# Kernel tuning notes

Hardware: AMD Instinct MI355X
Metric: run time of the kernel (lower is better)

## Reference

```python
import jax, jax.numpy as jnp
import numpy as np

N_GRAPHS = 512
NODES_PER_G = 200
EDGES_PER_G = 6400
N = N_GRAPHS * NODES_PER_G        # 102400 nodes
E = N_GRAPHS * EDGES_PER_G        # 3276800 edges
HID = 128
NCLS = 10


def _linear_params(key, fan_in, fan_out):
    # torch nn.Linear default init: U(-1/sqrt(fan_in), 1/sqrt(fan_in))
    s = 1.0 / np.sqrt(fan_in)
    kw, kb = jax.random.split(key)
    W = jax.random.uniform(kw, (fan_in, fan_out), minval=-s, maxval=s, dtype=jnp.float32)
    b = jax.random.uniform(kb, (fan_out,), minval=-s, maxval=s, dtype=jnp.float32)
    return W, b


def setup_inputs() -> dict:
    key = jax.random.key(0)
    ks = jax.random.split(key, 10)
    # edges are confined within each graph (DGL batched graph structure)
    g_off = (jnp.arange(E, dtype=jnp.int32) // EDGES_PER_G) * NODES_PER_G
    src = (g_off + jax.random.randint(ks[0], (E,), 0, NODES_PER_G)).astype(jnp.int32)
    dst = (g_off + jax.random.randint(ks[1], (E,), 0, NODES_PER_G)).astype(jnp.int32)
    W1, b1 = _linear_params(ks[2], 1, HID)
    W2, b2 = _linear_params(ks[3], HID, HID)
    Wa, ba = _linear_params(ks[4], HID, 512)
    Wb, bb = _linear_params(ks[5], 512, 1024)
    Wc, bc = _linear_params(ks[6], 1024, 1024)
    Wd, bd = _linear_params(ks[7], 1024, 512)
    We, be = _linear_params(ks[8], 512, NCLS)
    return dict(src=src, dst=dst, W1=W1, b1=b1, W2=W2, b2=b2,
                Wa=Wa, ba=ba, Wb=Wb, bb=bb, Wc=Wc, bc=bc,
                Wd=Wd, bd=bd, We=We, be=be)


def reference(src, dst, W1, b1, W2, b2, Wa, ba, Wb, bb, Wc, bc, Wd, bd, We, be):
    seg = jax.ops.segment_sum
    ones = jnp.ones((E,), jnp.float32)
    in_deg = seg(ones, dst, num_segments=N)    # [N]
    out_deg = seg(ones, src, num_segments=N)   # [N]
    # DGL GraphConv norm='both': degrees clamped to min 1
    inv_out = (1.0 / jnp.sqrt(jnp.maximum(out_deg, 1.0)))[:, None]
    inv_in = (1.0 / jnp.sqrt(jnp.maximum(in_deg, 1.0)))[:, None]

    def gconv(h, W, b):
        h = (h @ W) * inv_out                    # src-side normalize (weight applied first; same math)
        h = seg(h[src], dst, num_segments=N)     # gather + scatter-add aggregation
        return h * inv_in + b                    # dst-side normalize + bias

    h = in_deg[:, None]                          # input node features = in-degrees, [N,1]
    h = jax.nn.relu(gconv(h, W1, b1))
    h = jax.nn.relu(gconv(h, W2, b2))

    gid = jnp.arange(N, dtype=jnp.int32) // NODES_PER_G
    hg = seg(h, gid, num_segments=N_GRAPHS) / float(NODES_PER_G)  # mean readout, [G,HID]

    x = jax.nn.relu(hg @ Wa + ba)
    x = jax.nn.relu(x @ Wb + bb)
    x = jax.nn.relu(x @ Wc + bc)
    x = jax.nn.relu(x @ Wd + bd)
    return jax.nn.softmax(x @ We + be, axis=-1)  # nn.Softmax over class dim
```

## Files before the change

### kernel.cpp

```cpp
#include <hip/hip_runtime.h>
#include <stdint.h>

typedef unsigned short u16;
typedef unsigned int   u32;

#define NG   512
#define NPG  200
#define EPG  6400
#define NN   (NG*NPG)
#define NE_  (NG*EPG)
#define HID  128
#define KP   224
#define AP   232
#define ZP   136
#define RQ   64
#define QCAP 2048

__device__ __forceinline__ float bf2f(u16 b){ u32 u = ((u32)b) << 16; return __builtin_bit_cast(float, u); }
__device__ __forceinline__ u16 f2bf(float f){
    u32 u = __builtin_bit_cast(u32, f);
    u = (u + 0x7FFFu + ((u >> 16) & 1u)) >> 16;
    return (u16)u;
}

typedef __attribute__((ext_vector_type(8))) short bf16x8;
typedef __attribute__((ext_vector_type(4))) float f32x4;

enum : int {
  O_W1 = 0,        O_b1 = 128,      O_W2 = 256,      O_b2 = 16640,
  O_Wa = 16768,    O_ba = 82304,    O_Wb = 82816,    O_bb = 607104,
  O_Wc = 608128,   O_bc = 1656704,  O_Wd = 1657728,  O_bd = 2182016,
  O_We = 2182528,  O_be = 2187648,  O_END = 2187658
};

__global__ __launch_bounds__(128) void k_detect(const u16* __restrict__ w1bits,
                                                int* __restrict__ flag)
{
    __shared__ int cnt;
    const int tid = threadIdx.x;
    if (tid == 0) cnt = 0;
    __syncthreads();
    u16 u = w1bits[tid];
    int e = (u >> 7) & 0xFF;
    if (e >= 0x7F) atomicAdd(&cnt, 1);
    __syncthreads();
    if (tid == 0) *flag = (cnt > 4) ? 1 : 0;
}

struct Cvt { const void* src[14]; int off[15]; };

__global__ __launch_bounds__(256) void k_convert(Cvt c, float* __restrict__ dst,
                                                 const int* __restrict__ flag, int total)
{
    const int f = *flag;
    int i = blockIdx.x * 256 + threadIdx.x;
    if (i >= total) return;
    int t = 0;
    while (i >= c.off[t+1]) t++;
    int j = i - c.off[t];
    dst[i] = f ? ((const float*)c.src[t])[j] : bf2f(((const u16*)c.src[t])[j]);
}

__global__ __launch_bounds__(256) void k_w2t(const void* __restrict__ w2src,
                                             const float* __restrict__ w2canon,
                                             u16* __restrict__ W2T,
                                             float* __restrict__ hg,
                                             const int* __restrict__ flag)
{
    int i = blockIdx.x * 256 + threadIdx.x;
    if (i < HID*HID){
        int outc = i >> 7, inc = i & 127;
        int jsrc = inc*HID + outc;
        W2T[i] = (*flag) ? f2bf(w2canon[jsrc]) : ((const u16*)w2src)[jsrc];
    }
    #pragma unroll
    for (int k = 0; k < 4; k++){
        int j = blockIdx.x * 1024 + k*256 + threadIdx.x;
        if (j < NG*HID) hg[j] = 0.f;
    }
}

__global__ __launch_bounds__(256) void k_graph_l1(
    const int* __restrict__ src, const int* __restrict__ dst,
    const float* __restrict__ W1, const float* __restrict__ b1,
    float* __restrict__ invInG, u16* __restrict__ h1sT,
    u32* __restrict__ edgeBuf, int* __restrict__ cntQ)
{
    __shared__ u16 srcL[EPG];
    __shared__ u16 dstL[EPG];
    __shared__ int degIn[NPG];
    __shared__ int degOut[NPG];
    __shared__ int qcur[4];
    __shared__ float sValL[NPG], sAgg[NPG], iiL[NPG], ioL[NPG], tL[NPG];
    __shared__ float w1L[HID], b1L[HID];

    const int g = blockIdx.x, tid = threadIdx.x;

    if (tid < NPG){ degIn[tid] = 0; degOut[tid] = 0; sAgg[tid] = 0.f; }
    if (tid < HID){ w1L[tid] = W1[tid]; b1L[tid] = b1[tid]; }
    if (tid < 4) qcur[tid] = 0;
    __syncthreads();

    const int ebase = g * EPG;
    #pragma unroll
    for (int i = 0; i < EPG/256; i++){
        int e = i*256 + tid;
        int s = src[ebase + e] - g*NPG;
        int d = dst[ebase + e] - g*NPG;
        srcL[e] = (u16)s; dstL[e] = (u16)d;
        atomicAdd(&degOut[s], 1);
        atomicAdd(&degIn[d], 1);
    }
    __syncthreads();

    if (tid < NPG){
        int din = degIn[tid], dout = degOut[tid];
        float ii = rsqrtf(fmaxf((float)din, 1.f));
        float io = rsqrtf(fmaxf((float)dout, 1.f));
        iiL[tid] = ii; ioL[tid] = io;
        sValL[tid] = (float)din * io;
        invInG[g*NPG + tid] = ii;
    }
    __syncthreads();

    #pragma unroll
    for (int i = 0; i < EPG/256; i++){
        int e = i*256 + tid;
        int s = srcL[e], d = dstL[e];
        atomicAdd(&sAgg[d], sValL[s]);
        int q = (d * 41) >> 11;
        int pos = atomicAdd(&qcur[q], 1);
        if (pos < QCAP)
            edgeBuf[((size_t)(g*4 + q))*QCAP + pos] = (u32)s | ((u32)(d - q*50) << 16);
    }
    __syncthreads();

    if (tid < 4) cntQ[g*4 + tid] = (qcur[tid] < QCAP) ? qcur[tid] : QCAP;
    if (tid < NPG) tL[tid] = sAgg[tid] * iiL[tid];
    __syncthreads();

    const size_t base = (size_t)g * HID * KP;
    #pragma unroll 4
    for (int i = 0; i < HID*KP/256; i++){
        int idx = i*256 + tid;
        int c = idx / KP, v = idx - c*KP;
        u16 o = 0;
        if (v < NPG)
            o = f2bf(fmaxf(fmaf(tL[v], w1L[c], b1L[c]), 0.f) * ioL[v]);
        h1sT[base + idx] = o;
    }
}

__global__ __launch_bounds__(256, 4) void k_fused_graph(
    const u32* __restrict__ edgeBuf, const int* __restrict__ cntQ,
    const u16* __restrict__ h1sT, const u16* __restrict__ W2T,
    const float* __restrict__ invInG, const float* __restrict__ b2,
    float* __restrict__ hg)
{
    __shared__ __align__(16) u16 AZ[RQ*AP];
    __shared__ float invInL[RQ];
    __shared__ float b2L[HID];
    __shared__ float poolL[HID];

    const int bid = blockIdx.x, tid = threadIdx.x;
    const int g = bid >> 2, q = bid & 3;
    u32* az32 = (u32*)AZ;
    uint4* az4 = (uint4*)AZ;

    #pragma unroll
    for (int i = 0; i < 8; i++){
        int idx = i*256 + tid;
        if (idx < RQ*AP/8) az4[idx] = make_uint4(0,0,0,0);
    }
    if (tid < HID){ b2L[tid] = b2[tid]; poolL[tid] = 0.f; }
    if (tid < RQ) invInL[tid] = (tid < 50) ? invInG[g*NPG + q*50 + tid] : 0.f;
    __syncthreads();

    const int cnt = cntQ[bid];
    const u32* eb = edgeBuf + (size_t)bid * QCAP;
    for (int i = tid; i < cnt; i += 256){
        u32 e = eb[i];
        int s = e & 0xFFFF, dl = e >> 16;
        int idx = dl*AP + s;
        atomicAdd(&az32[idx >> 1], 1u << (16*(idx & 1)));
    }
    __syncthreads();

    for (int i = tid; i < RQ*AP/2; i += 256){
        u32 wv = az32[i];
        if (wv)
            az32[i] = (u32)f2bf((float)(wv & 0xFFFFu)) | ((u32)f2bf((float)(wv >> 16)) << 16);
    }
    __syncthreads();

    const int w = tid >> 6, lane = tid & 63;
    const int wm = w >> 1, wn = w & 1;
    const int lr = lane & 15, quad = lane >> 4;

    f32x4 acc[2][4];
    const f32x4 fz = {0.f, 0.f, 0.f, 0.f};
    #pragma unroll
    for (int mi = 0; mi < 2; mi++)
        #pragma unroll
        for (int nt = 0; nt < 4; nt++) acc[mi][nt] = fz;

    {
        const u16* Bg = h1sT + (size_t)g * HID * KP + (size_t)(wn*64) * KP;
        bf16x8 bcur[4], bnxt[4];
        #pragma unroll
        for (int nt = 0; nt < 4; nt++)
            bcur[nt] = *(const bf16x8*)&Bg[(nt*16 + lr)*KP + quad*8];
        for (int ks = 0; ks < 7; ks++){
            if (ks < 6){
                #pragma unroll
                for (int nt = 0; nt < 4; nt++)
                    bnxt[nt] = *(const bf16x8*)&Bg[(nt*16 + lr)*KP + (ks+1)*32 + quad*8];
            }
            bf16x8 af[2];
            #pragma unroll
            for (int mi = 0; mi < 2; mi++)
                af[mi] = *(const bf16x8*)&AZ[((wm*2 + mi)*16 + lr)*AP + ks*32 + quad*8];
            #pragma unroll
            for (int mi = 0; mi < 2; mi++)
                #pragma unroll
                for (int nt = 0; nt < 4; nt++)
                    acc[mi][nt] = __builtin_amdgcn_mfma_f32_16x16x32_bf16(
                        af[mi], bcur[nt], acc[mi][nt], 0, 0, 0);
            #pragma unroll
            for (int nt = 0; nt < 4; nt++) bcur[nt] = bnxt[nt];
        }
    }
    __syncthreads();

    #pragma unroll
    for (int mi = 0; mi < 2; mi++)
        #pragma unroll
        for (int nt = 0; nt < 4; nt++)
            #pragma unroll
            for (int r = 0; r < 4; r++){
                int v = (wm*2 + mi)*16 + quad*4 + r;
                int c = wn*64 + nt*16 + lr;
                AZ[v*ZP + c] = f2bf(acc[mi][nt][r]);
            }
    __syncthreads();

    #pragma unroll
    for (int mi = 0; mi < 2; mi++)
        #pragma unroll
        for (int nt = 0; nt < 4; nt++) acc[mi][nt] = fz;
    {
        const u16* Wg = W2T + (size_t)(wn*64) * HID;
        bf16x8 bcur[4], bnxt[4];
        #pragma unroll
        for (int nt = 0; nt < 4; nt++)
            bcur[nt] = *(const bf16x8*)&Wg[(nt*16 + lr)*HID + quad*8];
        for (int ks = 0; ks < 4; ks++){
            if (ks < 3){
                #pragma unroll
                for (int nt = 0; nt < 4; nt++)
                    bnxt[nt] = *(const bf16x8*)&Wg[(nt*16 + lr)*HID + (ks+1)*32 + quad*8];
            }
            bf16x8 af[2];
            #pragma unroll
            for (int mi = 0; mi < 2; mi++)
                af[mi] = *(const bf16x8*)&AZ[((wm*2 + mi)*16 + lr)*ZP + ks*32 + quad*8];
            #pragma unroll
            for (int mi = 0; mi < 2; mi++)
                #pragma unroll
                for (int nt = 0; nt < 4; nt++)
                    acc[mi][nt] = __builtin_amdgcn_mfma_f32_16x16x32_bf16(
                        af[mi], bcur[nt], acc[mi][nt], 0, 0, 0);
            #pragma unroll
            for (int nt = 0; nt < 4; nt++) bcur[nt] = bnxt[nt];
        }
    }

    #pragma unroll
    for (int mi = 0; mi < 2; mi++)
        #pragma unroll
        for (int nt = 0; nt < 4; nt++){
            int c = wn*64 + nt*16 + lr;
            float s = 0.f;
            #pragma unroll
            for (int r = 0; r < 4; r++){
                int v = (wm*2 + mi)*16 + quad*4 + r;
                if (v < 50)
                    s += fmaxf(fmaf(acc[mi][nt][r], invInL[v], b2L[c]), 0.f);
            }
            atomicAdd(&poolL[c], s);
        }
    __syncthreads();
    if (tid < HID) atomicAdd(&hg[(size_t)g*HID + tid], poolL[tid] * (1.f / NPG));
}

__global__ __launch_bounds__(256) void k_mlp(
    const float* __restrict__ A, const float* __restrict__ W,
    float* __restrict__ P, int K, int Nc, int chunk)
{
    constexpr int BM = 32, BN = 64, BK = 32;
    constexpr int LA = BM*BK/256;
    constexpr int LW = BK*BN/256;
    __shared__ __align__(16) float As[2][BK][BM + 4];
    __shared__ __align__(16) float Ws[2][BK][BN + 4];

    const int row0 = blockIdx.x * BM, col0 = blockIdx.y * BN, s = blockIdx.z;
    const int k0 = s * chunk;
    const int T = chunk / BK;
    const int tid = threadIdx.x;
    const int tm = (tid >> 4) * 2;
    const int tn = (tid & 15) * 4;

    float ra[LA], rw[LW];

    #pragma unroll
    for (int i = 0; i < LA; i++){
        int idx = i*256 + tid; int r = idx >> 5, kk = idx & 31;
        ra[i] = A[(size_t)(row0 + r)*K + k0 + kk];
    }
    #pragma unroll
    for (int i = 0; i < LW; i++){
        int idx = i*256 + tid; int kk = idx >> 6, c = idx & 63;
        rw[i] = W[(size_t)(k0 + kk)*Nc + col0 + c];
    }
    #pragma unroll
    for (int i = 0; i < LA; i++){
        int idx = i*256 + tid; int r = idx >> 5, kk = idx & 31;
        As[0][kk][r] = ra[i];
    }
    #pragma unroll
    for (int i = 0; i < LW; i++){
        int idx = i*256 + tid; int kk = idx >> 6, c = idx & 63;
        Ws[0][kk][c] = rw[i];
    }
    __syncthreads();

    float acc[2][4];
    #pragma unroll
    for (int i = 0; i < 2; i++)
        #pragma unroll
        for (int j = 0; j < 4; j++) acc[i][j] = 0.f;

    for (int t = 0; t < T-1; t++){
        const int buf = t & 1, nxt = buf ^ 1;
        const int kb = k0 + (t+1)*BK;
        #pragma unroll
        for (int i = 0; i < LA; i++){
            int idx = i*256 + tid; int r = idx >> 5, kk = idx & 31;
            ra[i] = A[(size_t)(row0 + r)*K + kb + kk];
        }
        #pragma unroll
        for (int i = 0; i < LW; i++){
            int idx = i*256 + tid; int kk = idx >> 6, c = idx & 63;
            rw[i] = W[(size_t)(kb + kk)*Nc + col0 + c];
        }
        #pragma unroll
        for (int kk = 0; kk < BK; kk++){
            float2 av = *(const float2*)&As[buf][kk][tm];
            float4 bv = *(const float4*)&Ws[buf][kk][tn];
            acc[0][0] = fmaf(av.x, bv.x, acc[0][0]); acc[0][1] = fmaf(av.x, bv.y, acc[0][1]);
            acc[0][2] = fmaf(av.x, bv.z, acc[0][2]); acc[0][3] = fmaf(av.x, bv.w, acc[0][3]);
            acc[1][0] = fmaf(av.y, bv.x, acc[1][0]); acc[1][1] = fmaf(av.y, bv.y, acc[1][1]);
            acc[1][2] = fmaf(av.y, bv.z, acc[1][2]); acc[1][3] = fmaf(av.y, bv.w, acc[1][3]);
        }
        #pragma unroll
        for (int i = 0; i < LA; i++){
            int idx = i*256 + tid; int r = idx >> 5, kk = idx & 31;
            As[nxt][kk][r] = ra[i];
        }
        #pragma unroll
        for (int i = 0; i < LW; i++){
            int idx = i*256 + tid; int kk = idx >> 6, c = idx & 63;
            Ws[nxt][kk][c] = rw[i];
        }
        __syncthreads();
    }
    {
        const int buf = (T-1) & 1;
        #pragma unroll
        for (int kk = 0; kk < BK; kk++){
            float2 av = *(const float2*)&As[buf][kk][tm];
            float4 bv = *(const float4*)&Ws[buf][kk][tn];
            acc[0][0] = fmaf(av.x, bv.x, acc[0][0]); acc[0][1] = fmaf(av.x, bv.y, acc[0][1]);
            acc[0][2] = fmaf(av.x, bv.z, acc[0][2]); acc[0][3] = fmaf(av.x, bv.w, acc[0][3]);
            acc[1][0] = fmaf(av.y, bv.x, acc[1][0]); acc[1][1] = fmaf(av.y, bv.y, acc[1][1]);
            acc[1][2] = fmaf(av.y, bv.z, acc[1][2]); acc[1][3] = fmaf(av.y, bv.w, acc[1][3]);
        }
    }

    float* Pd = P + (size_t)s * ((size_t)512 * Nc);
    #pragma unroll
    for (int i = 0; i < 2; i++){
        int r = row0 + tm + i;
        float4 v = { acc[i][0], acc[i][1], acc[i][2], acc[i][3] };
        *(float4*)&Pd[(size_t)r * Nc + col0 + tn] = v;
    }
}

__global__ __launch_bounds__(256) void k_reduce(
    const float* __restrict__ P, const float* __restrict__ bias,
    float* __restrict__ X, int MN, int Nc, int S)
{
    int e = blockIdx.x * 256 + threadIdx.x;
    int i0 = e * 4;
    if (i0 >= MN) return;
    float4 sum = *(const float4*)&P[i0];
    for (int s = 1; s < S; s++){
        float4 t = *(const float4*)&P[(size_t)s*MN + i0];
        sum.x += t.x; sum.y += t.y; sum.z += t.z; sum.w += t.w;
    }
    int col = i0 % Nc;
    float4 b = *(const float4*)&bias[col];
    sum.x = fmaxf(sum.x + b.x, 0.f);
    sum.y = fmaxf(sum.y + b.y, 0.f);
    sum.z = fmaxf(sum.z + b.z, 0.f);
    sum.w = fmaxf(sum.w + b.w, 0.f);
    *(float4*)&X[i0] = sum;
}

__global__ __launch_bounds__(64) void k_head(
    const float* __restrict__ X, const float* __restrict__ We,
    const float* __restrict__ be, void* __restrict__ out,
    const int* __restrict__ flag)
{
    const int g = blockIdx.x, lane = threadIdx.x;
    float part[10];
    #pragma unroll
    for (int c = 0; c < 10; c++) part[c] = 0.f;
    for (int k = lane; k < 512; k += 64){
        float x = X[(size_t)g*512 + k];
        #pragma unroll
        for (int c = 0; c < 10; c++) part[c] = fmaf(x, We[k*10 + c], part[c]);
    }
    #pragma unroll
    for (int c = 0; c < 10; c++){
        float v = part[c];
        for (int off = 32; off > 0; off >>= 1) v += __shfl_down(v, off);
        part[c] = v;
    }
    if (lane == 0){
        const int f = *flag;
        #pragma unroll
        for (int c = 0; c < 10; c++) part[c] += be[c];
        float m = part[0];
        #pragma unroll
        for (int c = 1; c < 10; c++) m = fmaxf(m, part[c]);
        float e[10], s = 0.f;
        #pragma unroll
        for (int c = 0; c < 10; c++){ e[c] = __expf(part[c] - m); s += e[c]; }
        float inv = 1.f / s;
        #pragma unroll
        for (int c = 0; c < 10; c++){
            float p = e[c] * inv;
            if (f) ((float*)out)[g*10 + c] = p;
            else   ((u16*)out)[g*10 + c]  = f2bf(p);
        }
    }
}

extern "C" void kernel_launch(void* const* d_in, const int* in_sizes, int n_in,
                              void* d_out, int out_size, void* d_ws, size_t ws_size,
                              hipStream_t stream)
{
    const int* src = (const int*)d_in[0];
    const int* dst = (const int*)d_in[1];

    char* ws = (char*)d_ws;
    size_t o = 0;
    int*   flag     = (int*)  (ws + o); o += 16;
    float* wcanon   = (float*)(ws + o); o += ((size_t)O_END * 4 + 15) & ~(size_t)15;
    u16*   W2T      = (u16*)  (ws + o); o += (size_t)HID * HID * 2;
    float* invIn    = (float*)(ws + o); o += (size_t)NN * 4;
    u32*   edgeBuf  = (u32*)  (ws + o); o += (size_t)NG * 4 * QCAP * 4;
    int*   cntQ     = (int*)  (ws + o); o += (size_t)NG * 4 * 4;
    u16*   h1sT     = (u16*)  (ws + o); o += (size_t)NG * HID * KP * 2;
    float* hg       = (float*)(ws + o); o += (size_t)NG * HID * 4;
    float* X1       = (float*)(ws + o); o += (size_t)NG * 512 * 4;
    float* X2       = (float*)(ws + o); o += (size_t)NG * 1024 * 4;
    float* X3       = (float*)(ws + o); o += (size_t)NG * 1024 * 4;
    float* X4       = (float*)(ws + o); o += (size_t)NG * 512 * 4;
    float* Pp       = (float*)h1sT;
    (void)ws_size; (void)in_sizes; (void)n_in; (void)out_size;

    k_detect<<<dim3(1), dim3(128), 0, stream>>>((const u16*)d_in[2], flag);

    Cvt cv;
    const int offs[15] = {O_W1,O_b1,O_W2,O_b2,O_Wa,O_ba,O_Wb,O_bb,O_Wc,O_bc,O_Wd,O_bd,O_We,O_be,O_END};
    for (int i = 0; i < 14; i++){ cv.src[i] = d_in[2 + i]; cv.off[i] = offs[i]; }
    cv.off[14] = offs[14];
    k_convert<<<dim3((O_END + 255)/256), dim3(256), 0, stream>>>(cv, wcanon, flag, O_END);
    k_w2t<<<dim3(64), dim3(256), 0, stream>>>(d_in[4], wcanon + O_W2, W2T, hg, flag);

    const float *W1 = wcanon+O_W1, *b1 = wcanon+O_b1, *b2 = wcanon+O_b2;
    const float *Wa = wcanon+O_Wa, *ba = wcanon+O_ba, *Wb = wcanon+O_Wb, *bb = wcanon+O_bb;
    const float *Wc = wcanon+O_Wc, *bc = wcanon+O_bc, *Wd = wcanon+O_Wd, *bd = wcanon+O_bd;
    const float *We = wcanon+O_We, *be = wcanon+O_be;

    k_graph_l1<<<dim3(NG), dim3(256), 0, stream>>>(
        src, dst, W1, b1, invIn, h1sT, edgeBuf, cntQ);

    k_fused_graph<<<dim3(NG*4), dim3(256), 0, stream>>>(
        edgeBuf, cntQ, h1sT, W2T, invIn, b2, hg);

    k_mlp<<<dim3(16, 8, 2),  dim3(256), 0, stream>>>(hg, Wa, Pp, 128, 512, 64);
    k_reduce<<<dim3(512*512/1024), dim3(256), 0, stream>>>(Pp, ba, X1, 512*512, 512, 2);
    k_mlp<<<dim3(16, 16, 4), dim3(256), 0, stream>>>(X1, Wb, Pp, 512, 1024, 128);
    k_reduce<<<dim3(512*1024/1024), dim3(256), 0, stream>>>(Pp, bb, X2, 512*1024, 1024, 4);
    k_mlp<<<dim3(16, 16, 4), dim3(256), 0, stream>>>(X2, Wc, Pp, 1024, 1024, 256);
    k_reduce<<<dim3(512*1024/1024), dim3(256), 0, stream>>>(Pp, bc, X3, 512*1024, 1024, 4);
    k_mlp<<<dim3(16, 8, 4),  dim3(256), 0, stream>>>(X3, Wd, Pp, 1024, 512, 256);
    k_reduce<<<dim3(512*512/1024), dim3(256), 0, stream>>>(Pp, bd, X4, 512*512, 512, 4);

    k_head<<<dim3(NG), dim3(64), 0, stream>>>(X4, We, be, d_out, flag);
}
```

Before: 293.2 us.

## Replace fp32 SIMT MLP GEMMs with bf16 split-precision MFMA kernels

Swaps the four fp32 FMA GEMM layers and their split-K reduce kernels for one MFMA kernel per layer. Activations are stored as hi/lo bf16 pairs and multiplied against a pre-transposed bf16 weight copy, which is built by a new transpose kernel. Split-K now happens inside the block and is reduced through shared memory, and bias plus ReLU are fused into the epilogue. This removes the reduce launches and the partial-sum traffic. In exchange, weights are rounded to bf16 and operands are read straight from global memory without LDS staging.

```diff
diff --git a/kernel.cpp b/kernel.cpp
--- a/kernel.cpp
+++ b/kernel.cpp
@@ -33,6 +33,14 @@
   O_We = 2182528,  O_be = 2187648,  O_END = 2187658
 };
 
+enum : int {
+  T_Wa = 0,
+  T_Wb = 65536,
+  T_Wc = 65536 + 524288,
+  T_Wd = 65536 + 524288 + 1048576,
+  T_END = 65536 + 524288 + 1048576 + 524288
+};
+
 __global__ __launch_bounds__(128) void k_detect(const u16* __restrict__ w1bits,
                                                 int* __restrict__ flag)
 {
@@ -78,6 +86,26 @@
         int j = blockIdx.x * 1024 + k*256 + threadIdx.x;
         if (j < NG*HID) hg[j] = 0.f;
     }
+}
+
+struct TD { const void* src; int coff; int logK; int N; int dst0; int dst1; };
+struct TD4 { TD t[4]; };
+
+__global__ __launch_bounds__(256) void k_wt(TD4 d, const float* __restrict__ canon,
+                                            u16* __restrict__ dst,
+                                            const int* __restrict__ flag, int total)
+{
+    const int f = *flag;
+    int i = blockIdx.x * 256 + threadIdx.x;
+    if (i >= total) return;
+    int t = 0;
+    while (i >= d.t[t].dst1) t++;
+    const TD& td = d.t[t];
+    int j = i - td.dst0;
+    int n = j >> td.logK;
+    int k = j & ((1 << td.logK) - 1);
+    int srcidx = k * td.N + n;
+    dst[i] = f ? f2bf(canon[td.coff + srcidx]) : ((const u16*)td.src)[srcidx];
 }
 
 __global__ __launch_bounds__(256) void k_graph_l1(
@@ -293,141 +321,92 @@
     if (tid < HID) atomicAdd(&hg[(size_t)g*HID + tid], poolL[tid] * (1.f / NPG));
 }
 
-__global__ __launch_bounds__(256) void k_mlp(
-    const float* __restrict__ A, const float* __restrict__ W,
-    float* __restrict__ P, int K, int Nc, int chunk)
-{
-    constexpr int BM = 32, BN = 64, BK = 32;
-    constexpr int LA = BM*BK/256;
-    constexpr int LW = BK*BN/256;
-    __shared__ __align__(16) float As[2][BK][BM + 4];
-    __shared__ __align__(16) float Ws[2][BK][BN + 4];
-
-    const int row0 = blockIdx.x * BM, col0 = blockIdx.y * BN, s = blockIdx.z;
-    const int k0 = s * chunk;
-    const int T = chunk / BK;
+template<int K, bool AF32>
+__global__ __launch_bounds__(512) void k_mlp3(
+    const void* __restrict__ Ahi_, const u16* __restrict__ Alo,
+    const u16* __restrict__ WT, const float* __restrict__ bias,
+    u16* __restrict__ Ohi, u16* __restrict__ Olo, int Nc)
+{
+    __shared__ float red[32][68];
+
     const int tid = threadIdx.x;
-    const int tm = (tid >> 4) * 2;
-    const int tn = (tid & 15) * 4;
-
-    float ra[LA], rw[LW];
-
-    #pragma unroll
-    for (int i = 0; i < LA; i++){
-        int idx = i*256 + tid; int r = idx >> 5, kk = idx & 31;
-        ra[i] = A[(size_t)(row0 + r)*K + k0 + kk];
-    }
-    #pragma unroll
-    for (int i = 0; i < LW; i++){
-        int idx = i*256 + tid; int kk = idx >> 6, c = idx & 63;
-        rw[i] = W[(size_t)(k0 + kk)*Nc + col0 + c];
-    }
-    #pragma unroll
-    for (int i = 0; i < LA; i++){
-        int idx = i*256 + tid; int r = idx >> 5, kk = idx & 31;
-        As[0][kk][r] = ra[i];
-    }
-    #pragma unroll
-    for (int i = 0; i < LW; i++){
-        int idx = i*256 + tid; int kk = idx >> 6, c = idx & 63;
-        Ws[0][kk][c] = rw[i];
-    }
-    __syncthreads();
-
-    float acc[2][4];
-    #pragma unroll
-    for (int i = 0; i < 2; i++)
-        #pragma unroll
-        for (int j = 0; j < 4; j++) acc[i][j] = 0.f;
-
-    for (int t = 0; t < T-1; t++){
-        const int buf = t & 1, nxt = buf ^ 1;
-        const int kb = k0 + (t+1)*BK;
-        #pragma unroll
-        for (int i = 0; i < LA; i++){
-            int idx = i*256 + tid; int r = idx >> 5, kk = idx & 31;
-            ra[i] = A[(size_t)(row0 + r)*K + kb + kk];
-        }
-        #pragma unroll
-        for (int i = 0; i < LW; i++){
-            int idx = i*256 + tid; int kk = idx >> 6, c = idx & 63;
-            rw[i] = W[(size_t)(kb + kk)*Nc + col0 + c];
-        }
-        #pragma unroll
-        for (int kk = 0; kk < BK; kk++){
-            float2 av = *(const float2*)&As[buf][kk][tm];
-            float4 bv = *(const float4*)&Ws[buf][kk][tn];
-            acc[0][0] = fmaf(av.x, bv.x, acc[0][0]); acc[0][1] = fmaf(av.x, bv.y, acc[0][1]);
-            acc[0][2] = fmaf(av.x, bv.z, acc[0][2]); acc[0][3] = fmaf(av.x, bv.w, acc[0][3]);
-            acc[1][0] = fmaf(av.y, bv.x, acc[1][0]); acc[1][1] = fmaf(av.y, bv.y, acc[1][1]);
-            acc[1][2] = fmaf(av.y, bv.z, acc[1][2]); acc[1][3] = fmaf(av.y, bv.w, acc[1][3]);
-        }
-        #pragma unroll
-        for (int i = 0; i < LA; i++){
-            int idx = i*256 + tid; int r = idx >> 5, kk = idx & 31;
-            As[nxt][kk][r] = ra[i];
-        }
-        #pragma unroll
-        for (int i = 0; i < LW; i++){
-            int idx = i*256 + tid; int kk = idx >> 6, c = idx & 63;
-            Ws[nxt][kk][c] = rw[i];
-        }
-        __syncthreads();
-    }
-    {
-        const int buf = (T-1) & 1;
-        #pragma unroll
-        for (int kk = 0; kk < BK; kk++){
-            float2 av = *(const float2*)&As[buf][kk][tm];
-            float4 bv = *(const float4*)&Ws[buf][kk][tn];
-            acc[0][0] = fmaf(av.x, bv.x, acc[0][0]); acc[0][1] = fmaf(av.x, bv.y, acc[0][1]);
-            acc[0][2] = fmaf(av.x, bv.z, acc[0][2]); acc[0][3] = fmaf(av.x, bv.w, acc[0][3]);
-            acc[1][0] = fmaf(av.y, bv.x, acc[1][0]); acc[1][1] = fmaf(av.y, bv.y, acc[1][1]);
-            acc[1][2] = fmaf(av.y, bv.z, acc[1][2]); acc[1][3] = fmaf(av.y, bv.w, acc[1][3]);
-        }
-    }
-
-    float* Pd = P + (size_t)s * ((size_t)512 * Nc);
-    #pragma unroll
-    for (int i = 0; i < 2; i++){
-        int r = row0 + tm + i;
-        float4 v = { acc[i][0], acc[i][1], acc[i][2], acc[i][3] };
-        *(float4*)&Pd[(size_t)r * Nc + col0 + tn] = v;
-    }
-}
-
-__global__ __launch_bounds__(256) void k_reduce(
-    const float* __restrict__ P, const float* __restrict__ bias,
-    float* __restrict__ X, int MN, int Nc, int S)
-{
-    int e = blockIdx.x * 256 + threadIdx.x;
-    int i0 = e * 4;
-    if (i0 >= MN) return;
-    float4 sum = *(const float4*)&P[i0];
-    for (int s = 1; s < S; s++){
-        float4 t = *(const float4*)&P[(size_t)s*MN + i0];
-        sum.x += t.x; sum.y += t.y; sum.z += t.z; sum.w += t.w;
-    }
-    int col = i0 % Nc;
-    float4 b = *(const float4*)&bias[col];
-    sum.x = fmaxf(sum.x + b.x, 0.f);
-    sum.y = fmaxf(sum.y + b.y, 0.f);
-    sum.z = fmaxf(sum.z + b.z, 0.f);
-    sum.w = fmaxf(sum.w + b.w, 0.f);
-    *(float4*)&X[i0] = sum;
+    const int w = tid >> 6, lane = tid & 63;
+    const int kz = w >> 2, wm = (w >> 1) & 1, wn = w & 1;
+    const int lr = lane & 15, quad = lane >> 4;
+    const int row0 = blockIdx.x * 32, col0 = blockIdx.y * 64;
+    const int m = row0 + wm*16 + lr;
+    constexpr int KH = K / 2;
+    const int k0 = kz * KH;
+
+    const float* Af = (const float*)Ahi_;
+    const u16*   Ah = (const u16*)Ahi_;
+
+    const f32x4 fz = {0.f, 0.f, 0.f, 0.f};
+    f32x4 acc[2] = {fz, fz};
+
+    #pragma unroll
+    for (int ks = 0; ks < KH/32; ks++){
+        const int kk = k0 + ks*32 + quad*8;
+        bf16x8 ahi, alo;
+        if constexpr (AF32){
+            float xs[8];
+            *(float4*)&xs[0] = *(const float4*)&Af[(size_t)m*K + kk];
+            *(float4*)&xs[4] = *(const float4*)&Af[(size_t)m*K + kk + 4];
+            #pragma unroll
+            for (int j = 0; j < 8; j++){
+                u16 hh = f2bf(xs[j]);
+                ahi[j] = (short)hh;
+                alo[j] = (short)f2bf(xs[j] - bf2f(hh));
+            }
+        } else {
+            ahi = *(const bf16x8*)&Ah[(size_t)m*K + kk];
+            alo = *(const bf16x8*)&Alo[(size_t)m*K + kk];
+        }
+        #pragma unroll
+        for (int nt = 0; nt < 2; nt++){
+            int n = col0 + wn*32 + nt*16 + lr;
+            bf16x8 b = *(const bf16x8*)&WT[(size_t)n*K + kk];
+            acc[nt] = __builtin_amdgcn_mfma_f32_16x16x32_bf16(ahi, b, acc[nt], 0, 0, 0);
+            acc[nt] = __builtin_amdgcn_mfma_f32_16x16x32_bf16(alo, b, acc[nt], 0, 0, 0);
+        }
+    }
+
+    if (kz == 1){
+        #pragma unroll
+        for (int nt = 0; nt < 2; nt++)
+            #pragma unroll
+            for (int r = 0; r < 4; r++)
+                red[wm*16 + quad*4 + r][wn*32 + nt*16 + lr] = acc[nt][r];
+    }
+    __syncthreads();
+    if (kz == 0){
+        #pragma unroll
+        for (int nt = 0; nt < 2; nt++)
+            #pragma unroll
+            for (int r = 0; r < 4; r++){
+                int rr = wm*16 + quad*4 + r;
+                int cc = wn*32 + nt*16 + lr;
+                float v = acc[nt][r] + red[rr][cc] + bias[col0 + cc];
+                v = fmaxf(v, 0.f);
+                u16 hh = f2bf(v);
+                size_t go = (size_t)(row0 + rr) * Nc + col0 + cc;
+                Ohi[go] = hh;
+                Olo[go] = f2bf(v - bf2f(hh));
+            }
+    }
 }
 
 __global__ __launch_bounds__(64) void k_head(
-    const float* __restrict__ X, const float* __restrict__ We,
-    const float* __restrict__ be, void* __restrict__ out,
-    const int* __restrict__ flag)
+    const u16* __restrict__ Xhi, const u16* __restrict__ Xlo,
+    const float* __restrict__ We, const float* __restrict__ be,
+    void* __restrict__ out, const int* __restrict__ flag)
 {
     const int g = blockIdx.x, lane = threadIdx.x;
     float part[10];
     #pragma unroll
     for (int c = 0; c < 10; c++) part[c] = 0.f;
     for (int k = lane; k < 512; k += 64){
-        float x = X[(size_t)g*512 + k];
+        float x = bf2f(Xhi[(size_t)g*512 + k]) + bf2f(Xlo[(size_t)g*512 + k]);
         #pragma unroll
         for (int c = 0; c < 10; c++) part[c] = fmaf(x, We[k*10 + c], part[c]);
     }
@@ -469,16 +448,20 @@
     int*   flag     = (int*)  (ws + o); o += 16;
     float* wcanon   = (float*)(ws + o); o += ((size_t)O_END * 4 + 15) & ~(size_t)15;
     u16*   W2T      = (u16*)  (ws + o); o += (size_t)HID * HID * 2;
+    u16*   WTa      = (u16*)  (ws + o); o += ((size_t)T_END * 2 + 15) & ~(size_t)15;
     float* invIn    = (float*)(ws + o); o += (size_t)NN * 4;
     u32*   edgeBuf  = (u32*)  (ws + o); o += (size_t)NG * 4 * QCAP * 4;
     int*   cntQ     = (int*)  (ws + o); o += (size_t)NG * 4 * 4;
     u16*   h1sT     = (u16*)  (ws + o); o += (size_t)NG * HID * KP * 2;
     float* hg       = (float*)(ws + o); o += (size_t)NG * HID * 4;
-    float* X1       = (float*)(ws + o); o += (size_t)NG * 512 * 4;
-    float* X2       = (float*)(ws + o); o += (size_t)NG * 1024 * 4;
-    float* X3       = (float*)(ws + o); o += (size_t)NG * 1024 * 4;
-    float* X4       = (float*)(ws + o); o += (size_t)NG * 512 * 4;
-    float* Pp       = (float*)h1sT;
+    u16*   X1hi     = (u16*)  (ws + o); o += (size_t)NG * 512 * 2;
+    u16*   X1lo     = (u16*)  (ws + o); o += (size_t)NG * 512 * 2;
+    u16*   X2hi     = (u16*)  (ws + o); o += (size_t)NG * 1024 * 2;
+    u16*   X2lo     = (u16*)  (ws + o); o += (size_t)NG * 1024 * 2;
+    u16*   X3hi     = (u16*)  (ws + o); o += (size_t)NG * 1024 * 2;
+    u16*   X3lo     = (u16*)  (ws + o); o += (size_t)NG * 1024 * 2;
+    u16*   X4hi     = (u16*)  (ws + o); o += (size_t)NG * 512 * 2;
+    u16*   X4lo     = (u16*)  (ws + o); o += (size_t)NG * 512 * 2;
     (void)ws_size; (void)in_sizes; (void)n_in; (void)out_size;
 
     k_detect<<<dim3(1), dim3(128), 0, stream>>>((const u16*)d_in[2], flag);
@@ -490,9 +473,15 @@
     k_convert<<<dim3((O_END + 255)/256), dim3(256), 0, stream>>>(cv, wcanon, flag, O_END);
     k_w2t<<<dim3(64), dim3(256), 0, stream>>>(d_in[4], wcanon + O_W2, W2T, hg, flag);
 
+    TD4 td;
+    td.t[0] = { d_in[6],  O_Wa, 7,  512,  T_Wa, T_Wb };
+    td.t[1] = { d_in[8],  O_Wb, 9,  1024, T_Wb, T_Wc };
+    td.t[2] = { d_in[10], O_Wc, 10, 1024, T_Wc, T_Wd };
+    td.t[3] = { d_in[12], O_Wd, 10, 512,  T_Wd, T_END };
+    k_wt<<<dim3((T_END + 255)/256), dim3(256), 0, stream>>>(td, wcanon, WTa, flag, T_END);
+
     const float *W1 = wcanon+O_W1, *b1 = wcanon+O_b1, *b2 = wcanon+O_b2;
-    const float *Wa = wcanon+O_Wa, *ba = wcanon+O_ba, *Wb = wcanon+O_Wb, *bb = wcanon+O_bb;
-    const float *Wc = wcanon+O_Wc, *bc = wcanon+O_bc, *Wd = wcanon+O_Wd, *bd = wcanon+O_bd;
+    const float *ba = wcanon+O_ba, *bb = wcanon+O_bb, *bc = wcanon+O_bc, *bd = wcanon+O_bd;
     const float *We = wcanon+O_We, *be = wcanon+O_be;
 
     k_graph_l1<<<dim3(NG), dim3(256), 0, stream>>>(
@@ -501,14 +490,10 @@
     k_fused_graph<<<dim3(NG*4), dim3(256), 0, stream>>>(
         edgeBuf, cntQ, h1sT, W2T, invIn, b2, hg);
 
-    k_mlp<<<dim3(16, 8, 2),  dim3(256), 0, stream>>>(hg, Wa, Pp, 128, 512, 64);
-    k_reduce<<<dim3(512*512/1024), dim3(256), 0, stream>>>(Pp, ba, X1, 512*512, 512, 2);
-    k_mlp<<<dim3(16, 16, 4), dim3(256), 0, stream>>>(X1, Wb, Pp, 512, 1024, 128);
-    k_reduce<<<dim3(512*1024/1024), dim3(256), 0, stream>>>(Pp, bb, X2, 512*1024, 1024, 4);
-    k_mlp<<<dim3(16, 16, 4), dim3(256), 0, stream>>>(X2, Wc, Pp, 1024, 1024, 256);
-    k_reduce<<<dim3(512*1024/1024), dim3(256), 0, stream>>>(Pp, bc, X3, 512*1024, 1024, 4);
-    k_mlp<<<dim3(16, 8, 4),  dim3(256), 0, stream>>>(X3, Wd, Pp, 1024, 512, 256);
-    k_reduce<<<dim3(512*512/1024), dim3(256), 0, stream>>>(Pp, bd, X4, 512*512, 512, 4);
-
-    k_head<<<dim3(NG), dim3(64), 0, stream>>>(X4, We, be, d_out, flag);
-}
+    k_mlp3<128,  true ><<<dim3(16, 8),  dim3(512), 0, stream>>>(hg,   nullptr, WTa + T_Wa, ba, X1hi, X1lo, 512);
+    k_mlp3<512,  false><<<dim3(16, 16), dim3(512), 0, stream>>>(X1hi, X1lo,    WTa + T_Wb, bb, X2hi, X2lo, 1024);
+    k_mlp3<1024, false><<<dim3(16, 16), dim3(512), 0, stream>>>(X2hi, X2lo,    WTa + T_Wc, bc, X3hi, X3lo, 1024);
+    k_mlp3<1024, false><<<dim3(16, 8),  dim3(512), 0, stream>>>(X3hi, X3lo,    WTa + T_Wd, bd, X4hi, X4lo, 512);
+
+    k_head<<<dim3(NG), dim3(64), 0, stream>>>(X4hi, X4lo, We, be, d_out, flag);
+}
```

After: 278.8 us. 4.9% less time.
